# Optimization experiments

Measured on AMD Instinct MI355X. Metric: run time of the kernel, lower is better.

Reference implementation:

```python
import jax, jax.numpy as jnp
import numpy as np

NEG_INF = -10000000.0


def setup_inputs() -> dict:
    key = jax.random.key(0)
    ks = jax.random.split(key, 9)
    B, S, H = 16, 2048, 1024
    std = 1.0 / np.sqrt(H)
    return {
        "queries": jax.random.normal(ks[0], (B, S, H), jnp.float32),
        "keys": jax.random.normal(ks[1], (B, S, H), jnp.float32),
        "values": jax.random.normal(ks[2], (B, S, H), jnp.float32),
        "Wq": jax.random.normal(ks[3], (H, H), jnp.float32) * std,
        "bq": jax.random.normal(ks[4], (H,), jnp.float32) * std,
        "Wk": jax.random.normal(ks[5], (H, H), jnp.float32) * std,
        "bk": jax.random.normal(ks[6], (H,), jnp.float32) * std,
        "Wv": jax.random.normal(ks[7], (H, H), jnp.float32) * std,
        "bv": jax.random.normal(ks[8], (H,), jnp.float32) * std,
    }


def reference(queries, keys, values, Wq, bq, Wk, bk, Wv, bv):
    H = queries.shape[-1]
    scale = jnp.asarray(1.0, queries.dtype) / jnp.sqrt(jnp.asarray(H, queries.dtype))
    # nn.Linear: x @ W.T + b
    q = queries @ Wq.T + bq          # [B, Q, H]
    k = keys @ Wk.T + bk             # [B, S, H]
    v = values @ Wv.T + bv           # [B, S, H]
    # torch: unnorm = k.bmm(q^T) -> [B, S, Q]; permuted to [B, Q, S] before softmax.
    scores = jnp.einsum('bqh,bsh->bqs', q, k) * scale   # [B, Q, S]
    Qlen, Slen = scores.shape[1], scores.shape[2]
    # tril(ones, diagonal=-1) on [S, Q]: entry (s, q) masked when s > q.
    # In the permuted [q, s] layout: mask where s > q (causal).
    mask = jnp.where(jnp.arange(Slen)[None, :] > jnp.arange(Qlen)[:, None],
                     jnp.asarray(NEG_INF, scores.dtype),
                     jnp.asarray(0.0, scores.dtype))
    attention_weights = jax.nn.softmax(scores + mask, axis=-1)  # [B, Q, S]
    context = jnp.einsum('bqs,bsh->bqh', attention_weights, v)  # [B, Q, H]
    # module returns attention_weights permuted back to [B, S, Q]
    return context, attention_weights.transpose(0, 2, 1)
```

## Files before the change

### kernel.cpp

```cpp
#include <hip/hip_runtime.h>
#include <hip/hip_bf16.h>
#include <cstdint>


typedef unsigned short u16;
typedef __bf16 bfrag __attribute__((ext_vector_type(8)));
typedef float f32x4 __attribute__((ext_vector_type(4)));

#define DEVI __device__ __forceinline__

DEVI u16 f2bf(float f) {
  unsigned u = __builtin_bit_cast(unsigned, f);
  u += 0x7FFFu + ((u >> 16) & 1u);
  return (u16)(u >> 16);
}

DEVI void g2l16(const void* g, void* l) {
  __builtin_amdgcn_global_load_lds(
      (const __attribute__((address_space(1))) void*)g,
      (__attribute__((address_space(3))) void*)l, 16, 0, 0);
}

__global__ void cast_f32_to_bf16(const float* __restrict__ in, u16* __restrict__ out, long n4) {
  long i = (long)blockIdx.x * blockDim.x + threadIdx.x;
  long stride = (long)gridDim.x * blockDim.x;
  for (long j = i; j < n4; j += stride) {
    float4 v = ((const float4*)in)[j];
    ushort4 o;
    o.x = f2bf(v.x); o.y = f2bf(v.y); o.z = f2bf(v.z); o.w = f2bf(v.w);
    ((ushort4*)out)[j] = o;
  }
}

template<int OUT_F32, int BIAS_MODE, int CAUSAL>
__global__ __launch_bounds__(512, 2)
void gemm_nt256(const u16* __restrict__ A, const u16* __restrict__ B,
                void* __restrict__ Cv, const float* __restrict__ bias,
                float scale, int K, long sA, long sB, long sC, int ldc,
                int gx, int gy)
{
  int nwg = gridDim.x * gridDim.y * gridDim.z;
  int hbid = blockIdx.x + gridDim.x * (blockIdx.y + gridDim.y * blockIdx.z);
  int cpx = nwg >> 3;
  int l = (hbid & 7) * cpx + (hbid >> 3);
  int bx = l % gx;
  int rest = l / gx;
  int by = rest % gy;
  int bz = rest / gy;

  long n0 = (long)bx * 256;
  long m0 = (long)by * 256;
  if (CAUSAL == 1 && m0 > n0 + 255) return;
  const u16* Ab = A + (long)bz * sA;
  const u16* Bb = B + (long)bz * sB;

  __shared__ __align__(16) u16 lA[2][256 * 64];
  __shared__ __align__(16) u16 lB[2][256 * 64];

  int tid = threadIdx.x;
  int lane = tid & 63;
  int wid = tid >> 6;
  int wr = wid >> 2;
  int wc = wid & 3;

  f32x4 acc[8][4] = {};

  int kmax = (CAUSAL == 2) ? ((K < m0 + 256) ? K : (int)(m0 + 256)) : K;
  int nkt = kmax >> 6;

  auto stage = [&](int kt, int bsel) {
    long k0 = (long)kt << 6;
    #pragma unroll
    for (int i = 0; i < 4; ++i) {
      int c = tid + (i << 9);
      int row = c >> 3;
      int sc = (c & 7) ^ (row & 7);
      g2l16(Ab + (m0 + row) * (long)K + k0 + (sc << 3), (char*)lA[bsel] + c * 16);
      g2l16(Bb + (n0 + row) * (long)K + k0 + (sc << 3), (char*)lB[bsel] + c * 16);
    }
  };

  stage(0, 0);
  __syncthreads();
  int cur = 0;
  for (int kt = 0; kt < nkt; ++kt) {
    if (kt + 1 < nkt) stage(kt + 1, cur ^ 1);
    const char* la = (const char*)lA[cur];
    const char* lb = (const char*)lB[cur];
    #pragma unroll
    for (int k2 = 0; k2 < 2; ++k2) {
      int kbc = (k2 << 2) + (lane >> 4);
      int rsel = lane & 15;
      bfrag af[8], bf[4];
      #pragma unroll
      for (int f = 0; f < 8; ++f) {
        int ra = wr * 128 + f * 16 + rsel;
        af[f] = *(const bfrag*)(la + ra * 128 + ((kbc ^ (ra & 7)) << 4));
      }
      #pragma unroll
      for (int f = 0; f < 4; ++f) {
        int rb = wc * 64 + f * 16 + rsel;
        bf[f] = *(const bfrag*)(lb + rb * 128 + ((kbc ^ (rb & 7)) << 4));
      }
      #pragma unroll
      for (int mi = 0; mi < 8; ++mi)
        #pragma unroll
        for (int ni = 0; ni < 4; ++ni)
          acc[mi][ni] = __builtin_amdgcn_mfma_f32_16x16x32_bf16(af[mi], bf[ni], acc[mi][ni], 0, 0, 0);
    }
    __syncthreads();
    cur ^= 1;
  }

  long cmb = m0 + wr * 128 + (lane >> 4) * 4;
  long cnb = n0 + wc * 64 + (lane & 15);
  #pragma unroll
  for (int mi = 0; mi < 8; ++mi) {
    #pragma unroll
    for (int ni = 0; ni < 4; ++ni) {
      f32x4 v = acc[mi][ni];
      long col = cnb + ni * 16;
      #pragma unroll
      for (int i = 0; i < 4; ++i) {
        long row = cmb + mi * 16 + i;
        float x = v[i] * scale;
        if (BIAS_MODE == 1) x += bias[col];
        if (BIAS_MODE == 2) x += bias[row];
        long cidx = (long)bz * sC + row * ldc + col;
        if (OUT_F32) ((float*)Cv)[cidx] = x;
        else         ((u16*)Cv)[cidx] = f2bf(x);
      }
    }
  }
}

__global__ __launch_bounds__(512)
void softmax_stats(const float* __restrict__ att, float* __restrict__ mo,
                   float* __restrict__ lo, int S) {
  int b  = blockIdx.y;
  int q0 = blockIdx.x * 64;
  int t  = threadIdx.x;
  int ql = t & 63;
  int grp = t >> 6;
  int q = q0 + ql;
  const float* a = att + (long)b * S * S + q;
  int send = q0 + 64;
  float m = -3.0e38f, l = 0.0f;
  for (int s = grp; s < send; s += 8) {
    float v = (s <= q) ? a[(long)s * S] : -3.0e38f;
    float mn = fmaxf(m, v);
    l = l * __expf(m - mn) + __expf(v - mn);
    m = mn;
  }
  __shared__ float sm[8][64], sl[8][64];
  sm[grp][ql] = m;
  sl[grp][ql] = l;
  __syncthreads();
  if (t < 64) {
    float M = sm[0][t];
    #pragma unroll
    for (int g = 1; g < 8; ++g) M = fmaxf(M, sm[g][t]);
    float L = 0.0f;
    #pragma unroll
    for (int g = 0; g < 8; ++g) L += sl[g][t] * __expf(sm[g][t] - M);
    mo[(long)b * S + q0 + t] = M;
    lo[(long)b * S + q0 + t] = L;
  }
}

__global__ void norm_transpose(float* __restrict__ att, const float* __restrict__ ms,
                               const float* __restrict__ ls, u16* __restrict__ probs, int S) {
  int b  = blockIdx.z;
  int q0 = blockIdx.x * 64;
  int s0 = blockIdx.y * 64;
  float* a = att + (long)b * S * S;
  u16* p = probs + (long)b * S * S;
  int tid = threadIdx.x;
  bool needp = s0 < ((q0 & ~255) + 256);

  if (s0 > q0 + 63) {
    float4 z = make_float4(0.f, 0.f, 0.f, 0.f);
    ushort4 zu; zu.x = zu.y = zu.z = zu.w = 0;
    #pragma unroll
    for (int it = 0; it < 4; ++it) {
      int j = tid + it * 256; int row = j >> 4; int c4 = (j & 15) * 4;
      *(float4*)&a[(long)(s0 + row) * S + q0 + c4] = z;
      if (needp) *(ushort4*)&p[(long)(q0 + row) * S + s0 + c4] = zu;
    }
    return;
  }

  __shared__ float t[64][65];
  __shared__ float lm[64], lr[64];
  if (tid < 64) {
    lm[tid] = ms[(long)b * S + q0 + tid];
    lr[tid] = 1.0f / ls[(long)b * S + q0 + tid];
  }
  __syncthreads();

  #pragma unroll
  for (int it = 0; it < 4; ++it) {
    int j = tid + it * 256; int row = j >> 4; int c4 = (j & 15) * 4;
    int s = s0 + row;
    float4 v = *(const float4*)&a[(long)s * S + q0 + c4];
    float vv[4] = {v.x, v.y, v.z, v.w};
    float oo[4];
    #pragma unroll
    for (int e = 0; e < 4; ++e) {
      int q = q0 + c4 + e;
      float pv = (s <= q) ? __expf(vv[e] - lm[c4 + e]) * lr[c4 + e] : 0.0f;
      oo[e] = pv;
      t[row][c4 + e] = pv;
    }
    float4 ov; ov.x = oo[0]; ov.y = oo[1]; ov.z = oo[2]; ov.w = oo[3];
    *(float4*)&a[(long)s * S + q0 + c4] = ov;
  }
  __syncthreads();

  #pragma unroll
  for (int it = 0; it < 4; ++it) {
    int j = tid + it * 256; int qrow = j >> 4; int sc4 = (j & 15) * 4;
    ushort4 ov;
    ov.x = f2bf(t[sc4 + 0][qrow]);
    ov.y = f2bf(t[sc4 + 1][qrow]);
    ov.z = f2bf(t[sc4 + 2][qrow]);
    ov.w = f2bf(t[sc4 + 3][qrow]);
    *(ushort4*)&p[(long)(q0 + qrow) * S + s0 + sc4] = ov;
  }
}

extern "C" void kernel_launch(void* const* d_in, const int* in_sizes, int n_in,
                              void* d_out, int out_size, void* d_ws, size_t ws_size,
                              hipStream_t stream) {
  const int B = 16, S = 2048, H = 1024;
  const long NE = (long)B * S * H;
  const float* Q  = (const float*)d_in[0];
  const float* Kk = (const float*)d_in[1];
  const float* V  = (const float*)d_in[2];
  const float* Wq = (const float*)d_in[3];
  const float* bq = (const float*)d_in[4];
  const float* Wk = (const float*)d_in[5];
  const float* bk = (const float*)d_in[6];
  const float* Wv = (const float*)d_in[7];
  const float* bv = (const float*)d_in[8];

  char* ws = (char*)d_ws;
  u16* xq    = (u16*)ws;
  u16* xk    = (u16*)(ws + (64L << 20));
  u16* xv    = (u16*)(ws + (128L << 20));
  u16* qb    = (u16*)(ws + (192L << 20));
  u16* kb    = (u16*)ws;
  u16* vT    = (u16*)(ws + (64L << 20));
  u16* probs = (u16*)(ws + (128L << 20));
  u16* Wqb   = (u16*)(ws + (256L << 20));
  u16* Wkb   = (u16*)(ws + (256L << 20) + (2L << 20));
  u16* Wvb   = (u16*)(ws + (256L << 20) + (4L << 20));
  float* mbuf = (float*)(ws + (256L << 20) + (6L << 20));
  float* lbuf = (float*)(ws + (256L << 20) + (6L << 20) + (1L << 17));

  float* ctx = (float*)d_out;
  float* att = (float*)d_out + NE;

  cast_f32_to_bf16<<<2048, 256, 0, stream>>>(Q,  xq, NE >> 2);
  cast_f32_to_bf16<<<2048, 256, 0, stream>>>(Kk, xk, NE >> 2);
  cast_f32_to_bf16<<<2048, 256, 0, stream>>>(V,  xv, NE >> 2);
  cast_f32_to_bf16<<<512, 256, 0, stream>>>(Wq, Wqb, ((long)H * H) >> 2);
  cast_f32_to_bf16<<<512, 256, 0, stream>>>(Wk, Wkb, ((long)H * H) >> 2);
  cast_f32_to_bf16<<<512, 256, 0, stream>>>(Wv, Wvb, ((long)H * H) >> 2);

  gemm_nt256<0, 1, 0><<<dim3(4, 128, 1), 512, 0, stream>>>(
      xq, Wqb, qb, bq, 1.0f, H, 0, 0, 0, H, 4, 128);
  gemm_nt256<0, 1, 0><<<dim3(4, 128, 1), 512, 0, stream>>>(
      xk, Wkb, kb, bk, 1.0f, H, 0, 0, 0, H, 4, 128);
  gemm_nt256<0, 2, 0><<<dim3(8, 4, 16), 512, 0, stream>>>(
      Wvb, xv, vT, bv, 1.0f, H, 0, (long)S * H, (long)H * S, S, 8, 4);

  gemm_nt256<1, 0, 1><<<dim3(8, 8, 16), 512, 0, stream>>>(
      kb, qb, att, nullptr, 0.03125f, H, (long)S * H, (long)S * H,
      (long)S * S, S, 8, 8);

  softmax_stats<<<dim3(32, 16), 512, 0, stream>>>(att, mbuf, lbuf, S);

  norm_transpose<<<dim3(32, 32, 16), 256, 0, stream>>>(att, mbuf, lbuf, probs, S);

  gemm_nt256<1, 0, 2><<<dim3(4, 8, 16), 512, 0, stream>>>(
      probs, vT, ctx, nullptr, 1.0f, S, (long)S * S, (long)H * S,
      (long)S * H, H, 4, 8);
}
```

Measured before the change: 815.1 us.

## Replace double-buffered GEMM K-loop with 4-stage ring and manual vmcnt waits

The GEMM main loop moves from a 2-buffer, K=64 tile scheme to a 4-deep ring of K=32 tiles. Three tiles are prefetched ahead, and the loop waits with explicit s_waitcnt vmcnt counts, raw s_barrier and sched_barrier. It also raises wave priority around the MFMA block. The goal is to hide global-to-LDS load latency behind more outstanding loads and to avoid the full __syncthreads drain. In exchange it drops the XOR swizzle, so LDS bank conflicts may rise with the 64-byte row stride, and it doubles the loop iteration and barrier count.

```diff
diff --git a/kernel.cpp b/kernel.cpp
--- a/kernel.cpp
+++ b/kernel.cpp
@@ -8,6 +8,8 @@
 typedef float f32x4 __attribute__((ext_vector_type(4)));
 
 #define DEVI __device__ __forceinline__
+#define SBAR() __builtin_amdgcn_s_barrier()
+#define SCHED0() __builtin_amdgcn_sched_barrier(0)
 
 DEVI u16 f2bf(float f) {
   unsigned u = __builtin_bit_cast(unsigned, f);
@@ -54,8 +56,7 @@
   const u16* Ab = A + (long)bz * sA;
   const u16* Bb = B + (long)bz * sB;
 
-  __shared__ __align__(16) u16 lA[2][256 * 64];
-  __shared__ __align__(16) u16 lB[2][256 * 64];
+  __shared__ __align__(16) u16 ring[4][2][256 * 32];
 
   int tid = threadIdx.x;
   int lane = tid & 63;
@@ -66,50 +67,64 @@
   f32x4 acc[8][4] = {};
 
   int kmax = (CAUSAL == 2) ? ((K < m0 + 256) ? K : (int)(m0 + 256)) : K;
-  int nkt = kmax >> 6;
-
-  auto stage = [&](int kt, int bsel) {
-    long k0 = (long)kt << 6;
-    #pragma unroll
-    for (int i = 0; i < 4; ++i) {
+  int nkt = kmax >> 5;
+
+  auto stage = [&](int kt, int s) {
+    long k0 = (long)kt << 5;
+    u16* dA = &ring[s][0][0];
+    u16* dB = &ring[s][1][0];
+    #pragma unroll
+    for (int i = 0; i < 2; ++i) {
       int c = tid + (i << 9);
-      int row = c >> 3;
-      int sc = (c & 7) ^ (row & 7);
-      g2l16(Ab + (m0 + row) * (long)K + k0 + (sc << 3), (char*)lA[bsel] + c * 16);
-      g2l16(Bb + (n0 + row) * (long)K + k0 + (sc << 3), (char*)lB[bsel] + c * 16);
+      int row = c >> 2;
+      int cc = c & 3;
+      g2l16(Ab + (m0 + row) * (long)K + k0 + (cc << 3), (char*)dA + c * 16);
+    }
+    #pragma unroll
+    for (int i = 0; i < 2; ++i) {
+      int c = tid + (i << 9);
+      int row = c >> 2;
+      int cc = c & 3;
+      g2l16(Bb + (n0 + row) * (long)K + k0 + (cc << 3), (char*)dB + c * 16);
     }
   };
 
   stage(0, 0);
-  __syncthreads();
-  int cur = 0;
-  for (int kt = 0; kt < nkt; ++kt) {
-    if (kt + 1 < nkt) stage(kt + 1, cur ^ 1);
-    const char* la = (const char*)lA[cur];
-    const char* lb = (const char*)lB[cur];
-    #pragma unroll
-    for (int k2 = 0; k2 < 2; ++k2) {
-      int kbc = (k2 << 2) + (lane >> 4);
-      int rsel = lane & 15;
-      bfrag af[8], bf[4];
+  stage(1, 1);
+  stage(2, 2);
+
+  for (int t = 0; t < nkt; ++t) {
+    if (t + 3 < nkt) stage(t + 3, (t + 3) & 3);
+    SCHED0();
+    int rem = nkt - 1 - t;
+    if (rem >= 3)      asm volatile("s_waitcnt vmcnt(12)" ::: "memory");
+    else if (rem == 2) asm volatile("s_waitcnt vmcnt(8)" ::: "memory");
+    else if (rem == 1) asm volatile("s_waitcnt vmcnt(4)" ::: "memory");
+    else               asm volatile("s_waitcnt vmcnt(0)" ::: "memory");
+    SBAR();
+    SCHED0();
+
+    const char* la = (const char*)&ring[t & 3][0][0];
+    const char* lb = (const char*)&ring[t & 3][1][0];
+    int kc = (lane >> 4) << 4;
+    int rsel = lane & 15;
+    bfrag af[8], bf[4];
+    #pragma unroll
+    for (int f = 0; f < 8; ++f)
+      af[f] = *(const bfrag*)(la + (wr * 128 + f * 16 + rsel) * 64 + kc);
+    #pragma unroll
+    for (int f = 0; f < 4; ++f)
+      bf[f] = *(const bfrag*)(lb + (wc * 64 + f * 16 + rsel) * 64 + kc);
+
+    __builtin_amdgcn_s_setprio(1);
+    #pragma unroll
+    for (int mi = 0; mi < 8; ++mi)
       #pragma unroll
-      for (int f = 0; f < 8; ++f) {
-        int ra = wr * 128 + f * 16 + rsel;
-        af[f] = *(const bfrag*)(la + ra * 128 + ((kbc ^ (ra & 7)) << 4));
-      }
-      #pragma unroll
-      for (int f = 0; f < 4; ++f) {
-        int rb = wc * 64 + f * 16 + rsel;
-        bf[f] = *(const bfrag*)(lb + rb * 128 + ((kbc ^ (rb & 7)) << 4));
-      }
-      #pragma unroll
-      for (int mi = 0; mi < 8; ++mi)
-        #pragma unroll
-        for (int ni = 0; ni < 4; ++ni)
-          acc[mi][ni] = __builtin_amdgcn_mfma_f32_16x16x32_bf16(af[mi], bf[ni], acc[mi][ni], 0, 0, 0);
-    }
-    __syncthreads();
-    cur ^= 1;
+      for (int ni = 0; ni < 4; ++ni)
+        acc[mi][ni] = __builtin_amdgcn_mfma_f32_16x16x32_bf16(af[mi], bf[ni], acc[mi][ni], 0, 0, 0);
+    __builtin_amdgcn_s_setprio(0);
+    SCHED0();
+    SBAR();
   }
 
   long cmb = m0 + wr * 128 + (lane >> 4) * 4;
```

After: 867.6 us. +6.4%, slower.

## Shrink GEMM tiles to 128x128 with 256 threads and drop LDS double buffering

Applied to the files above, without the earlier changes.

Replaces the 256x256, 512-thread GEMM kernel with a 128x128, 256-thread version that uses a single LDS buffer and synchronizes before and after each K step, instead of prefetching the next tile. The smaller tiles raise block count and occupancy and make the causal skipping finer-grained. The causal PV GEMM also reverses its row order so the longest (bottom) rows are scheduled first. The costs are lost global-to-LDS load/compute overlap, more redundant operand traffic from smaller tiles, and an extra barrier per K step.

```diff
diff --git a/kernel.cpp b/kernel.cpp
--- a/kernel.cpp
+++ b/kernel.cpp
@@ -33,8 +33,8 @@
 }
 
 template<int OUT_F32, int BIAS_MODE, int CAUSAL>
-__global__ __launch_bounds__(512, 2)
-void gemm_nt256(const u16* __restrict__ A, const u16* __restrict__ B,
+__global__ __launch_bounds__(256)
+void gemm_nt128(const u16* __restrict__ A, const u16* __restrict__ B,
                 void* __restrict__ Cv, const float* __restrict__ bias,
                 float scale, int K, long sA, long sB, long sC, int ldc,
                 int gx, int gy)
@@ -47,75 +47,66 @@
   int rest = l / gx;
   int by = rest % gy;
   int bz = rest / gy;
-
-  long n0 = (long)bx * 256;
-  long m0 = (long)by * 256;
-  if (CAUSAL == 1 && m0 > n0 + 255) return;
+  if (CAUSAL == 2) by = (gy - 1) - by;
+
+  long n0 = (long)bx * 128;
+  long m0 = (long)by * 128;
+  if (CAUSAL == 1 && m0 > n0 + 127) return;
   const u16* Ab = A + (long)bz * sA;
   const u16* Bb = B + (long)bz * sB;
 
-  __shared__ __align__(16) u16 lA[2][256 * 64];
-  __shared__ __align__(16) u16 lB[2][256 * 64];
+  __shared__ __align__(16) u16 lA[128 * 64];
+  __shared__ __align__(16) u16 lB[128 * 64];
 
   int tid = threadIdx.x;
   int lane = tid & 63;
   int wid = tid >> 6;
-  int wr = wid >> 2;
-  int wc = wid & 3;
-
-  f32x4 acc[8][4] = {};
-
-  int kmax = (CAUSAL == 2) ? ((K < m0 + 256) ? K : (int)(m0 + 256)) : K;
+  int wr = wid >> 1, wc = wid & 1;
+
+  f32x4 acc[4][4] = {};
+
+  int kmax = (CAUSAL == 2) ? ((K < m0 + 128) ? K : (int)(m0 + 128)) : K;
   int nkt = kmax >> 6;
 
-  auto stage = [&](int kt, int bsel) {
+  for (int kt = 0; kt < nkt; ++kt) {
     long k0 = (long)kt << 6;
     #pragma unroll
     for (int i = 0; i < 4; ++i) {
-      int c = tid + (i << 9);
+      int c = tid + (i << 8);
       int row = c >> 3;
       int sc = (c & 7) ^ (row & 7);
-      g2l16(Ab + (m0 + row) * (long)K + k0 + (sc << 3), (char*)lA[bsel] + c * 16);
-      g2l16(Bb + (n0 + row) * (long)K + k0 + (sc << 3), (char*)lB[bsel] + c * 16);
-    }
-  };
-
-  stage(0, 0);
-  __syncthreads();
-  int cur = 0;
-  for (int kt = 0; kt < nkt; ++kt) {
-    if (kt + 1 < nkt) stage(kt + 1, cur ^ 1);
-    const char* la = (const char*)lA[cur];
-    const char* lb = (const char*)lB[cur];
+      g2l16(Ab + (m0 + row) * (long)K + k0 + (sc << 3), (char*)lA + c * 16);
+      g2l16(Bb + (n0 + row) * (long)K + k0 + (sc << 3), (char*)lB + c * 16);
+    }
+    __syncthreads();
     #pragma unroll
     for (int k2 = 0; k2 < 2; ++k2) {
       int kbc = (k2 << 2) + (lane >> 4);
       int rsel = lane & 15;
-      bfrag af[8], bf[4];
-      #pragma unroll
-      for (int f = 0; f < 8; ++f) {
-        int ra = wr * 128 + f * 16 + rsel;
-        af[f] = *(const bfrag*)(la + ra * 128 + ((kbc ^ (ra & 7)) << 4));
+      bfrag af[4], bf[4];
+      #pragma unroll
+      for (int f = 0; f < 4; ++f) {
+        int ra = wr * 64 + f * 16 + rsel;
+        af[f] = *(const bfrag*)((const char*)lA + ra * 128 + ((kbc ^ (ra & 7)) << 4));
       }
       #pragma unroll
       for (int f = 0; f < 4; ++f) {
         int rb = wc * 64 + f * 16 + rsel;
-        bf[f] = *(const bfrag*)(lb + rb * 128 + ((kbc ^ (rb & 7)) << 4));
+        bf[f] = *(const bfrag*)((const char*)lB + rb * 128 + ((kbc ^ (rb & 7)) << 4));
       }
       #pragma unroll
-      for (int mi = 0; mi < 8; ++mi)
+      for (int mi = 0; mi < 4; ++mi)
         #pragma unroll
         for (int ni = 0; ni < 4; ++ni)
           acc[mi][ni] = __builtin_amdgcn_mfma_f32_16x16x32_bf16(af[mi], bf[ni], acc[mi][ni], 0, 0, 0);
     }
     __syncthreads();
-    cur ^= 1;
-  }
-
-  long cmb = m0 + wr * 128 + (lane >> 4) * 4;
+  }
+
+  long cmb = m0 + wr * 64 + (lane >> 4) * 4;
   long cnb = n0 + wc * 64 + (lane & 15);
   #pragma unroll
-  for (int mi = 0; mi < 8; ++mi) {
+  for (int mi = 0; mi < 4; ++mi) {
     #pragma unroll
     for (int ni = 0; ni < 4; ++ni) {
       f32x4 v = acc[mi][ni];
@@ -176,7 +167,7 @@
   float* a = att + (long)b * S * S;
   u16* p = probs + (long)b * S * S;
   int tid = threadIdx.x;
-  bool needp = s0 < ((q0 & ~255) + 256);
+  bool needp = s0 < ((q0 & ~127) + 128);
 
   if (s0 > q0 + 63) {
     float4 z = make_float4(0.f, 0.f, 0.f, 0.f);
@@ -268,22 +259,22 @@
   cast_f32_to_bf16<<<512, 256, 0, stream>>>(Wk, Wkb, ((long)H * H) >> 2);
   cast_f32_to_bf16<<<512, 256, 0, stream>>>(Wv, Wvb, ((long)H * H) >> 2);
 
-  gemm_nt256<0, 1, 0><<<dim3(4, 128, 1), 512, 0, stream>>>(
-      xq, Wqb, qb, bq, 1.0f, H, 0, 0, 0, H, 4, 128);
-  gemm_nt256<0, 1, 0><<<dim3(4, 128, 1), 512, 0, stream>>>(
-      xk, Wkb, kb, bk, 1.0f, H, 0, 0, 0, H, 4, 128);
-  gemm_nt256<0, 2, 0><<<dim3(8, 4, 16), 512, 0, stream>>>(
-      Wvb, xv, vT, bv, 1.0f, H, 0, (long)S * H, (long)H * S, S, 8, 4);
-
-  gemm_nt256<1, 0, 1><<<dim3(8, 8, 16), 512, 0, stream>>>(
+  gemm_nt128<0, 1, 0><<<dim3(8, 256, 1), 256, 0, stream>>>(
+      xq, Wqb, qb, bq, 1.0f, H, 0, 0, 0, H, 8, 256);
+  gemm_nt128<0, 1, 0><<<dim3(8, 256, 1), 256, 0, stream>>>(
+      xk, Wkb, kb, bk, 1.0f, H, 0, 0, 0, H, 8, 256);
+  gemm_nt128<0, 2, 0><<<dim3(16, 8, 16), 256, 0, stream>>>(
+      Wvb, xv, vT, bv, 1.0f, H, 0, (long)S * H, (long)H * S, S, 16, 8);
+
+  gemm_nt128<1, 0, 1><<<dim3(16, 16, 16), 256, 0, stream>>>(
       kb, qb, att, nullptr, 0.03125f, H, (long)S * H, (long)S * H,
-      (long)S * S, S, 8, 8);
+      (long)S * S, S, 16, 16);
 
   softmax_stats<<<dim3(32, 16), 512, 0, stream>>>(att, mbuf, lbuf, S);
 
   norm_transpose<<<dim3(32, 32, 16), 256, 0, stream>>>(att, mbuf, lbuf, probs, S);
 
-  gemm_nt256<1, 0, 2><<<dim3(4, 8, 16), 512, 0, stream>>>(
+  gemm_nt128<1, 0, 2><<<dim3(8, 16, 16), 256, 0, stream>>>(
       probs, vT, ctx, nullptr, 1.0f, S, (long)S * S, (long)H * S,
-      (long)S * H, H, 4, 8);
-}
+      (long)S * H, H, 8, 16);
+}
```

Measured after the change: 930.1 us. 1.14x slower.
